# Optimization experiments

Hardware: AMD Instinct MI355X
Metric: run time of the kernel (lower is better)

Reference implementation:

```python
import jax, jax.numpy as jnp
import numpy as np

WIDTH = 256
HEAD = 16
SCALE = 2
G = WIDTH // HEAD          # 16 groups
NH = G * SCALE             # 32 kernelized heads
EPS = 1e-5
N_NODES = 20000
B_GRAPHS = 1024


def setup_inputs() -> dict:
    key = jax.random.key(0)
    ks = jax.random.split(key, 10)
    x = jax.random.normal(ks[0], (N_NODES, WIDTH), jnp.float32)
    x_res = jax.random.normal(ks[1], (B_GRAPHS, NH, HEAD, HEAD), jnp.float32)
    batch = jnp.sort(jax.random.randint(ks[2], (N_NODES,), 0, B_GRAPHS)).astype(jnp.int64)
    w_pre = jax.random.normal(ks[3], (WIDTH, WIDTH), jnp.float32) * 0.02
    b_pre = jnp.zeros((WIDTH,), jnp.float32)
    # grouped 1x1 convs: [groups, width_scale, head_out, head_in]
    wq = jax.random.normal(ks[4], (G, SCALE, HEAD, HEAD), jnp.float32) * 0.02
    wk = jax.random.normal(ks[5], (G, SCALE, HEAD, HEAD), jnp.float32) * 0.02
    wv = jax.random.normal(ks[6], (G, SCALE, HEAD, HEAD), jnp.float32) * 0.02
    w_post = jax.random.normal(ks[7], (WIDTH, WIDTH * SCALE), jnp.float32) * 0.02
    b_post = jnp.zeros((WIDTH,), jnp.float32)
    log_scale = jnp.full((WIDTH,), np.log(0.01), jnp.float32)
    return {"x": x, "x_res": x_res, "batch": batch, "batch_size": B_GRAPHS,
            "w_pre": w_pre, "b_pre": b_pre, "wq": wq, "wk": wk, "wv": wv,
            "w_post": w_post, "b_post": b_post, "log_scale": log_scale}


def reference(x, x_res, batch, batch_size, w_pre, b_pre, wq, wk, wv, w_post, b_post, log_scale):
    n = x.shape[0]
    # pre: 1x1 conv (= linear) + GroupNorm(affine=False); L=1 so normalize over
    # each group's width_head channels.
    y = x @ w_pre.T + b_pre                       # [N, width]
    yg = y.reshape(n, G, HEAD)                    # [N, G, Hd]
    mu = yg.mean(-1, keepdims=True)
    var = yg.var(-1, keepdims=True)               # biased, as in GroupNorm
    yn = (yg - mu) / jnp.sqrt(var + EPS)          # [N, G, Hd]

    inv_sqrt_h = 1.0 / np.sqrt(HEAD)
    # grouped convs -> kernelized q,k (exp) and v
    xq = jnp.exp(jnp.einsum('ngi,gsoi->ngso', yn, wq) * inv_sqrt_h).reshape(n, NH, HEAD)
    xk = jnp.exp(jnp.einsum('ngi,gsoi->ngso', yn, wk) * inv_sqrt_h).reshape(n, NH, HEAD)
    xv = jnp.einsum('ngi,gsoi->ngso', yn, wv).reshape(n, NH, HEAD)

    # outer product k (x) v then scatter-sum over graphs  [B, NH, Hd, Hd]
    kv = jnp.einsum('bnh,bnv->bnhv', xk, xv)
    kv_sum = jax.ops.segment_sum(kv, batch, num_segments=batch_size) + x_res
    x_res_out = kv_sum

    # per-graph key sum, gathered back to nodes
    k_sum = jax.ops.segment_sum(xk, batch, num_segments=batch_size)[batch]  # [N, NH, Hd]
    denom = jnp.einsum('bnh,bnh->bn', xq, k_sum)                            # [N, NH]
    qn = xq / denom[:, :, None]

    out = jnp.einsum('bnh,bnhv->bnv', qn, kv_sum[batch]).reshape(n, WIDTH * SCALE)
    out = jnp.exp(log_scale) * (out @ w_post.T + b_post)                    # [N, width]
    return (out, x_res_out)
```

## Files before the change

### kernel.cpp

```cpp
#include <hip/hip_runtime.h>
#include <stdint.h>

typedef unsigned int u32;
typedef unsigned short u16;
typedef __attribute__((ext_vector_type(8))) short v8s;
typedef __attribute__((ext_vector_type(4))) float v4f;

#define GN_EPS 1e-5f

__device__ __forceinline__ float bflo(u32 u){ return __uint_as_float(u << 16); }
__device__ __forceinline__ float bfhi(u32 u){ return __uint_as_float(u & 0xffff0000u); }
__device__ __forceinline__ u16 f2bf(float f){
  u32 x = __float_as_uint(f);
  u32 r = (x + 0x7fffu + ((x >> 16) & 1u)) >> 16;
  return (u16)r;
}
__device__ __forceinline__ u32 pack2(float a, float b){
  return (u32)f2bf(a) | ((u32)f2bf(b) << 16);
}
__device__ __forceinline__ void unpack8(const uint4 u, float* f){
  f[0]=bflo(u.x); f[1]=bfhi(u.x); f[2]=bflo(u.y); f[3]=bfhi(u.y);
  f[4]=bflo(u.z); f[5]=bfhi(u.z); f[6]=bflo(u.w); f[7]=bfhi(u.w);
}
__device__ __forceinline__ uint4 loadpack8(const float* __restrict__ p){
  float4 a = *(const float4*)p, b = *(const float4*)(p + 4);
  return make_uint4(pack2(a.x,a.y),pack2(a.z,a.w),pack2(b.x,b.y),pack2(b.z,b.w));
}

__device__ __forceinline__ int getb(const int* __restrict__ b, int is64, int i){
  return b[is64 ? 2*i : i];
}

__global__ __launch_bounds__(256) void k_detect(
    const int* __restrict__ batch, int n, int* __restrict__ flags)
{
  int i = blockIdx.x*256 + threadIdx.x;
  int bad = 0;
  if (i < n - 1 && batch[i] > batch[i + 1]) bad = 1;
  if (__builtin_amdgcn_ballot_w64(bad) != 0 && (threadIdx.x & 63) == 0)
    atomicOr(&flags[0], 1);
}

__global__ __launch_bounds__(256) void k_bounds(
    const int* __restrict__ batch, const int* __restrict__ flags,
    int N, int B, int* __restrict__ bounds)
{
  int i = blockIdx.x*256 + threadIdx.x;
  if (i >= N) return;
  const int is64 = flags[0];
  int b = getb(batch, is64, i);
  int prev = (i == 0) ? -1 : getb(batch, is64, i - 1);
  for (int g = prev + 1; g <= b; g++) bounds[g] = i;
  if (i == N - 1)
    for (int g = b + 1; g <= B; g++) bounds[g] = N;
}

__global__ __launch_bounds__(256) void k_pre(
    const float* __restrict__ x, const float* __restrict__ wpre,
    const float* __restrict__ bpre, u16* __restrict__ y, int N, int nbm)
{
  __shared__ __align__(16) u16 As[128*40];
  __shared__ __align__(16) u16 Bs[64*40];
  const int t = threadIdx.x;
  const int bm = blockIdx.x % nbm;
  const int bn = blockIdx.x / nbm;
  const int m_base = bm*128, n_base = bn*64;
  const int w = t >> 6, lane = t & 63;
  const int wr = (w >> 1)*64, wc = (w & 1)*32;
  const int fr = lane & 15, fk = lane >> 4;
  const int arow = t >> 1, acol = (t & 1)*16;
  const int brow = t >> 2, bcol = (t & 3)*8;

  v4f acc[4][2];
#pragma unroll
  for (int i = 0; i < 4; i++)
#pragma unroll
    for (int j = 0; j < 2; j++) acc[i][j] = (v4f){0.f,0.f,0.f,0.f};

  for (int k0 = 0; k0 < 256; k0 += 32) {
    __syncthreads();
    {
      int gm = m_base + arow;
      uint4 a0 = make_uint4(0u,0u,0u,0u), a1 = make_uint4(0u,0u,0u,0u);
      if (gm < N) {
        a0 = loadpack8(x + (size_t)gm*256 + k0 + acol);
        a1 = loadpack8(x + (size_t)gm*256 + k0 + acol + 8);
      }
      *(uint4*)&As[arow*40 + acol]     = a0;
      *(uint4*)&As[arow*40 + acol + 8] = a1;
      uint4 bv = loadpack8(wpre + (size_t)(n_base + brow)*256 + k0 + bcol);
      *(uint4*)&Bs[brow*40 + bcol] = bv;
    }
    __syncthreads();
    v8s b0 = *(const v8s*)&Bs[(wc      + fr)*40 + fk*8];
    v8s b1 = *(const v8s*)&Bs[(wc + 16 + fr)*40 + fk*8];
#pragma unroll
    for (int mi = 0; mi < 4; mi++) {
      v8s a = *(const v8s*)&As[(wr + mi*16 + fr)*40 + fk*8];
      acc[mi][0] = __builtin_amdgcn_mfma_f32_16x16x32_bf16(a,b0,acc[mi][0],0,0,0);
      acc[mi][1] = __builtin_amdgcn_mfma_f32_16x16x32_bf16(a,b1,acc[mi][1],0,0,0);
    }
  }
#pragma unroll
  for (int nj = 0; nj < 2; nj++) {
    int col = n_base + wc + nj*16 + fr;
    float bpv = bpre[col];
#pragma unroll
    for (int mi = 0; mi < 4; mi++) {
#pragma unroll
      for (int r = 0; r < 4; r++) {
        int row = m_base + wr + mi*16 + fk*4 + r;
        if (row < N) y[(size_t)row*256 + col] = f2bf(acc[mi][nj][r] + bpv);
      }
    }
  }
}

__global__ __launch_bounds__(256) void k_gnqkv(
    const u16* __restrict__ y, const float* __restrict__ wq,
    const float* __restrict__ wk, const float* __restrict__ wv,
    u16* __restrict__ qo, u16* __restrict__ ko, u16* __restrict__ vo, int N)
{
  __shared__ __align__(16) float wL[3*512];
  const int t = threadIdx.x;
  const int g = blockIdx.x & 15;
  const int c = blockIdx.x >> 4;
  {
    const float* srcs[3] = {wq, wk, wv};
#pragma unroll
    for (int tz = 0; tz < 3; tz++) {
      wL[tz*512 + t]       = srcs[tz][g*512 + t];
      wL[tz*512 + t + 256] = srcs[tz][g*512 + t + 256];
    }
  }
  __syncthreads();
  const int node = c*256 + t;
  if (node >= N) return;

  const u16* yp = y + (size_t)node*256 + g*16;
  uint4 Y0 = *(const uint4*)yp;
  uint4 Y1 = *(const uint4*)(yp + 8);
  float a[16]; unpack8(Y0, a); unpack8(Y1, a + 8);
  float mu = 0.f;
#pragma unroll
  for (int i = 0; i < 16; i++) mu += a[i];
  mu *= 0.0625f;
  float s2 = 0.f;
#pragma unroll
  for (int i = 0; i < 16; i++) { float d = a[i]-mu; s2 = fmaf(d,d,s2); }
  float inv = rsqrtf(s2*0.0625f + GN_EPS);
  float yn[16];
#pragma unroll
  for (int i = 0; i < 16; i++) yn[i] = (a[i]-mu)*inv;

  u16* outs[3] = {qo, ko, vo};
#pragma unroll
  for (int tz = 0; tz < 3; tz++) {
#pragma unroll
    for (int s = 0; s < 2; s++) {
      u32 p[8];
#pragma unroll
      for (int o = 0; o < 16; o++) {
        const float* row = &wL[tz*512 + (s*16 + o)*16];
        float4 W0 = *(const float4*)row;
        float4 W1 = *(const float4*)(row + 4);
        float4 W2 = *(const float4*)(row + 8);
        float4 W3 = *(const float4*)(row + 12);
        float w[16] = {W0.x,W0.y,W0.z,W0.w,W1.x,W1.y,W1.z,W1.w,
                       W2.x,W2.y,W2.z,W2.w,W3.x,W3.y,W3.z,W3.w};
        float d = 0.f;
#pragma unroll
        for (int i = 0; i < 16; i++) d = fmaf(yn[i], w[i], d);
        if (tz < 2) d = __expf(d*0.25f);
        if (o & 1) p[o>>1] |= (u32)f2bf(d) << 16;
        else       p[o>>1]  = (u32)f2bf(d);
      }
      u16* dst = outs[tz] + (size_t)node*512 + g*32 + s*16;
      *(uint4*)dst       = make_uint4(p[0],p[1],p[2],p[3]);
      *(uint4*)(dst + 8) = make_uint4(p[4],p[5],p[6],p[7]);
    }
  }
}

__global__ __launch_bounds__(512) void k_segatt(
    const u16* __restrict__ xk, const u16* __restrict__ xv,
    const u16* __restrict__ xq, const float* __restrict__ xres,
    const int* __restrict__ bounds,
    float* __restrict__ out1, u16* __restrict__ att, int N)
{
  __shared__ __align__(16) float red[512*20];
  __shared__ __align__(16) float kspart[512];
  __shared__ __align__(16) u16 kvs[32*280];
  __shared__ float kss[32*17];
  const int b = blockIdx.x, t = threadIdx.x;
  const int lo = bounds[b], hi = bounds[b+1];
  const int half = t >> 8;
  const int nh = (t >> 3) & 31, hp = t & 7;

  float kv[2][16];
#pragma unroll
  for (int r = 0; r < 2; r++)
#pragma unroll
    for (int v = 0; v < 16; v++) kv[r][v] = 0.f;
  float ks0 = 0.f, ks1 = 0.f;

  const size_t koff = (size_t)nh*16 + 2*hp;
  const size_t voff = (size_t)nh*16;
  int node = lo + half;
  for (; node + 2 < hi; node += 4) {
    u32  kw0 = *(const u32*) (xk + (size_t)node*512 + koff);
    uint4 Va0 = *(const uint4*)(xv + (size_t)node*512 + voff);
    uint4 Va1 = *(const uint4*)(xv + (size_t)node*512 + voff + 8);
    u32  kw1 = *(const u32*) (xk + (size_t)(node+2)*512 + koff);
    uint4 Vb0 = *(const uint4*)(xv + (size_t)(node+2)*512 + voff);
    uint4 Vb1 = *(const uint4*)(xv + (size_t)(node+2)*512 + voff + 8);
    float a0 = bflo(kw0), a1 = bfhi(kw0);
    float b0 = bflo(kw1), b1 = bfhi(kw1);
    float va[16], vb[16];
    unpack8(Va0, va); unpack8(Va1, va + 8);
    unpack8(Vb0, vb); unpack8(Vb1, vb + 8);
    ks0 += a0 + b0; ks1 += a1 + b1;
#pragma unroll
    for (int v = 0; v < 16; v++) {
      kv[0][v] = fmaf(a0, va[v], kv[0][v]);
      kv[1][v] = fmaf(a1, va[v], kv[1][v]);
      kv[0][v] = fmaf(b0, vb[v], kv[0][v]);
      kv[1][v] = fmaf(b1, vb[v], kv[1][v]);
    }
  }
  if (node < hi) {
    u32  kw = *(const u32*) (xk + (size_t)node*512 + koff);
    uint4 V0 = *(const uint4*)(xv + (size_t)node*512 + voff);
    uint4 V1 = *(const uint4*)(xv + (size_t)node*512 + voff + 8);
    float k0 = bflo(kw), k1 = bfhi(kw);
    float vf[16]; unpack8(V0, vf); unpack8(V1, vf + 8);
    ks0 += k0; ks1 += k1;
#pragma unroll
    for (int v = 0; v < 16; v++) {
      kv[0][v] = fmaf(k0, vf[v], kv[0][v]);
      kv[1][v] = fmaf(k1, vf[v], kv[1][v]);
    }
  }

  if (half == 0) {
#pragma unroll
    for (int r = 0; r < 2; r++) {
      float* rp = &red[(nh*16 + 2*hp + r)*20];
      *(float4*)rp       = make_float4(kv[r][0], kv[r][1], kv[r][2], kv[r][3]);
      *(float4*)(rp + 4) = make_float4(kv[r][4], kv[r][5], kv[r][6], kv[r][7]);
      *(float4*)(rp + 8) = make_float4(kv[r][8], kv[r][9], kv[r][10],kv[r][11]);
      *(float4*)(rp + 12)= make_float4(kv[r][12],kv[r][13],kv[r][14],kv[r][15]);
    }
    kspart[nh*16 + 2*hp]     = ks0;
    kspart[nh*16 + 2*hp + 1] = ks1;
  }
  __syncthreads();

  if (half == 1) {
#pragma unroll
    for (int r = 0; r < 2; r++) {
      const float* rp = &red[(nh*16 + 2*hp + r)*20];
      float4 R0 = *(const float4*)rp;
      float4 R1 = *(const float4*)(rp + 4);
      float4 R2 = *(const float4*)(rp + 8);
      float4 R3 = *(const float4*)(rp + 12);
      kv[r][0] += R0.x; kv[r][1] += R0.y; kv[r][2] += R0.z; kv[r][3] += R0.w;
      kv[r][4] += R1.x; kv[r][5] += R1.y; kv[r][6] += R1.z; kv[r][7] += R1.w;
      kv[r][8] += R2.x; kv[r][9] += R2.y; kv[r][10]+= R2.z; kv[r][11]+= R2.w;
      kv[r][12]+= R3.x; kv[r][13]+= R3.y; kv[r][14]+= R3.z; kv[r][15]+= R3.w;
    }
    ks0 += kspart[nh*16 + 2*hp];
    ks1 += kspart[nh*16 + 2*hp + 1];
    kss[nh*17 + 2*hp]     = ks0;
    kss[nh*17 + 2*hp + 1] = ks1;

#pragma unroll
    for (int r = 0; r < 2; r++) {
      int h = 2*hp + r;
      size_t idx = ((size_t)(b*32 + nh)*16 + h)*16;
      const float* xp = xres + idx;
      float4 X0 = *(const float4*)xp;
      float4 X1 = *(const float4*)(xp + 4);
      float4 X2 = *(const float4*)(xp + 8);
      float4 X3 = *(const float4*)(xp + 12);
      float xf[16] = {X0.x,X0.y,X0.z,X0.w,X1.x,X1.y,X1.z,X1.w,
                      X2.x,X2.y,X2.z,X2.w,X3.x,X3.y,X3.z,X3.w};
      float o[16];
#pragma unroll
      for (int j = 0; j < 16; j++) o[j] = kv[r][j] + xf[j];
      float* op = out1 + idx;
      *(float4*)op        = make_float4(o[0],o[1],o[2],o[3]);
      *(float4*)(op + 4)  = make_float4(o[4],o[5],o[6],o[7]);
      *(float4*)(op + 8)  = make_float4(o[8],o[9],o[10],o[11]);
      *(float4*)(op + 12) = make_float4(o[12],o[13],o[14],o[15]);
      u16* lp = &kvs[nh*280 + h*16];
      *(uint4*)lp       = make_uint4(pack2(o[0],o[1]),  pack2(o[2],o[3]),
                                     pack2(o[4],o[5]),  pack2(o[6],o[7]));
      *(uint4*)(lp + 8) = make_uint4(pack2(o[8],o[9]),  pack2(o[10],o[11]),
                                     pack2(o[12],o[13]),pack2(o[14],o[15]));
    }
  }
  __syncthreads();

  const int nh2 = t & 31, ns = t >> 5;
  for (int n0 = lo; n0 < hi; n0 += 16) {
    int nodei = n0 + ns;
    if (nodei >= hi) continue;
    const u16* qp = xq + (size_t)nodei*512 + nh2*16;
    uint4 Q0 = *(const uint4*)qp;
    uint4 Q1 = *(const uint4*)(qp + 8);
    float q[16]; unpack8(Q0, q); unpack8(Q1, q + 8);
    const float* ksp = &kss[nh2*17];
    float denom = 0.f;
#pragma unroll
    for (int i = 0; i < 16; i++) denom = fmaf(q[i], ksp[i], denom);
    float inv = 1.0f / fmaxf(denom, 1e-20f);
    float a[16];
#pragma unroll
    for (int v = 0; v < 16; v++) a[v] = 0.f;
    const u16* kvp = &kvs[nh2*280];
#pragma unroll
    for (int h = 0; h < 16; h++) {
      float qh = q[h] * inv;
      uint4 W0 = *(const uint4*)(kvp + h*16);
      uint4 W1 = *(const uint4*)(kvp + h*16 + 8);
      float w[16]; unpack8(W0, w); unpack8(W1, w + 8);
#pragma unroll
      for (int v = 0; v < 16; v++) a[v] = fmaf(qh, w[v], a[v]);
    }
    u32 p[8];
#pragma unroll
    for (int j = 0; j < 8; j++) p[j] = pack2(a[2*j], a[2*j+1]);
    u16* dst = att + (size_t)nodei*512 + nh2*16;
    *(uint4*)dst       = make_uint4(p[0],p[1],p[2],p[3]);
    *(uint4*)(dst + 8) = make_uint4(p[4],p[5],p[6],p[7]);
  }
}

__global__ __launch_bounds__(256) void k_post(
    const u16* __restrict__ att, const float* __restrict__ wpost,
    const float* __restrict__ bpost, const float* __restrict__ ls,
    float* __restrict__ out0, int N, int nbm)
{
  __shared__ __align__(16) u16 As[128*40];
  __shared__ __align__(16) u16 Bs[64*40];
  const int t = threadIdx.x;
  const int bm = blockIdx.x % nbm;
  const int bn = blockIdx.x / nbm;
  const int m_base = bm*128, n_base = bn*64;
  const int w = t >> 6, lane = t & 63;
  const int wr = (w >> 1)*64, wc = (w & 1)*32;
  const int fr = lane & 15, fk = lane >> 4;
  const int arow = t >> 1, acol = (t & 1)*16;
  const int brow = t >> 2, bcol = (t & 3)*8;

  v4f acc[4][2];
#pragma unroll
  for (int i = 0; i < 4; i++)
#pragma unroll
    for (int j = 0; j < 2; j++) acc[i][j] = (v4f){0.f,0.f,0.f,0.f};

  for (int k0 = 0; k0 < 512; k0 += 32) {
    __syncthreads();
    {
      int gm = m_base + arow;
      uint4 a0 = make_uint4(0u,0u,0u,0u), a1 = make_uint4(0u,0u,0u,0u);
      if (gm < N) {
        a0 = *(const uint4*)(att + (size_t)gm*512 + k0 + acol);
        a1 = *(const uint4*)(att + (size_t)gm*512 + k0 + acol + 8);
      }
      *(uint4*)&As[arow*40 + acol]     = a0;
      *(uint4*)&As[arow*40 + acol + 8] = a1;
      uint4 bv = loadpack8(wpost + (size_t)(n_base + brow)*512 + k0 + bcol);
      *(uint4*)&Bs[brow*40 + bcol] = bv;
    }
    __syncthreads();
    v8s b0 = *(const v8s*)&Bs[(wc      + fr)*40 + fk*8];
    v8s b1 = *(const v8s*)&Bs[(wc + 16 + fr)*40 + fk*8];
#pragma unroll
    for (int mi = 0; mi < 4; mi++) {
      v8s a = *(const v8s*)&As[(wr + mi*16 + fr)*40 + fk*8];
      acc[mi][0] = __builtin_amdgcn_mfma_f32_16x16x32_bf16(a,b0,acc[mi][0],0,0,0);
      acc[mi][1] = __builtin_amdgcn_mfma_f32_16x16x32_bf16(a,b1,acc[mi][1],0,0,0);
    }
  }
#pragma unroll
  for (int nj = 0; nj < 2; nj++) {
    int col = n_base + wc + nj*16 + fr;
    float bpv = bpost[col];
    float e   = __expf(ls[col]);
#pragma unroll
    for (int mi = 0; mi < 4; mi++) {
#pragma unroll
      for (int r = 0; r < 4; r++) {
        int row = m_base + wr + mi*16 + fk*4 + r;
        if (row < N) out0[(size_t)row*256 + col] = e*(acc[mi][nj][r] + bpv);
      }
    }
  }
}

extern "C" void kernel_launch(void* const* d_in, const int* in_sizes, int n_in,
                              void* d_out, int out_size, void* d_ws, size_t ws_size,
                              hipStream_t stream)
{
  const float* x     = (const float*)d_in[0];
  const float* xres  = (const float*)d_in[1];
  const int*   batch = (const int*)d_in[2];
  const float* wpre  = (const float*)d_in[4];
  const float* bpre  = (const float*)d_in[5];
  const float* wq    = (const float*)d_in[6];
  const float* wk    = (const float*)d_in[7];
  const float* wv    = (const float*)d_in[8];
  const float* wpost = (const float*)d_in[9];
  const float* bpost = (const float*)d_in[10];
  const float* ls    = (const float*)d_in[11];

  const int N = in_sizes[0] / 256;
  const int B = in_sizes[1] / 8192;
  const int nbm = (N + 127) / 128;
  const int nchunk = (N + 255) / 256;

  char* ws = (char*)d_ws;
  size_t off = 0;
  int*   flags  = (int*)(ws + off); off += 256;
  int*   bounds = (int*)(ws + off); off += ((size_t)B + 64) * 4;
  u16*   y      = (u16*)(ws + off);  off += (size_t)N * 512;
  u16*   att    = (u16*)(ws + off);  off += (size_t)N * 1024;
  u16*   q      = (u16*)(ws + off);  off += (size_t)N * 1024;
  u16*   kten   = (u16*)(ws + off);  off += (size_t)N * 1024;
  u16*   vten   = (u16*)(ws + off);  off += (size_t)N * 1024;

  float* out0 = (float*)d_out;
  float* out1 = out0 + (size_t)N * 256;

  hipMemsetAsync(flags, 0, 4, stream);
  k_detect<<<nchunk,         256, 0, stream>>>(batch, N, flags);
  k_bounds<<<nchunk,         256, 0, stream>>>(batch, flags, N, B, bounds);
  k_pre   <<<nbm * 4,        256, 0, stream>>>(x, wpre, bpre, y, N, nbm);
  k_gnqkv <<<nchunk * 16,    256, 0, stream>>>(y, wq, wk, wv, q, kten, vten, N);
  k_segatt<<<B,              512, 0, stream>>>(kten, vten, q, xres, bounds,
                                               out1, att, N);
  k_post  <<<nbm * 4,        256, 0, stream>>>(att, wpost, bpost, ls, out0, N, nbm);
}
```

Baseline: 133.1 us.

## Remap segment KV reduction to one row per thread, drop shared-memory split reduction

The per-graph KV accumulation no longer splits nodes across two thread halves that are later combined through a 40KB shared reduction buffer. Each of the 512 threads now owns one (head, key-dim) row and walks every node of the graph, so the shared buffers and one barrier disappear. This frees LDS, which may allow more resident blocks, and removes the cross-half combine step. In exchange each thread runs twice as many serial node iterations, and the key loads become 2-byte scalar reads instead of paired 4-byte reads.

```diff
diff --git a/kernel.cpp b/kernel.cpp
--- a/kernel.cpp
+++ b/kernel.cpp
@@ -10,6 +10,7 @@
 
 __device__ __forceinline__ float bflo(u32 u){ return __uint_as_float(u << 16); }
 __device__ __forceinline__ float bfhi(u32 u){ return __uint_as_float(u & 0xffff0000u); }
+__device__ __forceinline__ float bf1(u16 u){ return __uint_as_float((u32)u << 16); }
 __device__ __forceinline__ u16 f2bf(float f){
   u32 x = __float_as_uint(f);
   u32 r = (x + 0x7fffu + ((x >> 16) & 1u)) >> 16;
@@ -188,117 +189,73 @@
     const int* __restrict__ bounds,
     float* __restrict__ out1, u16* __restrict__ att, int N)
 {
-  __shared__ __align__(16) float red[512*20];
-  __shared__ __align__(16) float kspart[512];
   __shared__ __align__(16) u16 kvs[32*280];
   __shared__ float kss[32*17];
   const int b = blockIdx.x, t = threadIdx.x;
   const int lo = bounds[b], hi = bounds[b+1];
-  const int half = t >> 8;
-  const int nh = (t >> 3) & 31, hp = t & 7;
-
-  float kv[2][16];
-#pragma unroll
-  for (int r = 0; r < 2; r++)
-#pragma unroll
-    for (int v = 0; v < 16; v++) kv[r][v] = 0.f;
-  float ks0 = 0.f, ks1 = 0.f;
-
-  const size_t koff = (size_t)nh*16 + 2*hp;
+  const int nh = t >> 4, d = t & 15;
+
+  float kv[16];
+#pragma unroll
+  for (int v = 0; v < 16; v++) kv[v] = 0.f;
+  float ks = 0.f;
+
+  const size_t koff = (size_t)nh*16 + d;
   const size_t voff = (size_t)nh*16;
-  int node = lo + half;
-  for (; node + 2 < hi; node += 4) {
-    u32  kw0 = *(const u32*) (xk + (size_t)node*512 + koff);
+  int node = lo;
+  for (; node + 1 < hi; node += 2) {
+    u16  ka  = xk[(size_t)node*512 + koff];
     uint4 Va0 = *(const uint4*)(xv + (size_t)node*512 + voff);
     uint4 Va1 = *(const uint4*)(xv + (size_t)node*512 + voff + 8);
-    u32  kw1 = *(const u32*) (xk + (size_t)(node+2)*512 + koff);
-    uint4 Vb0 = *(const uint4*)(xv + (size_t)(node+2)*512 + voff);
-    uint4 Vb1 = *(const uint4*)(xv + (size_t)(node+2)*512 + voff + 8);
-    float a0 = bflo(kw0), a1 = bfhi(kw0);
-    float b0 = bflo(kw1), b1 = bfhi(kw1);
+    u16  kb  = xk[(size_t)(node+1)*512 + koff];
+    uint4 Vb0 = *(const uint4*)(xv + (size_t)(node+1)*512 + voff);
+    uint4 Vb1 = *(const uint4*)(xv + (size_t)(node+1)*512 + voff + 8);
+    float k0 = bf1(ka), k1 = bf1(kb);
     float va[16], vb[16];
     unpack8(Va0, va); unpack8(Va1, va + 8);
     unpack8(Vb0, vb); unpack8(Vb1, vb + 8);
-    ks0 += a0 + b0; ks1 += a1 + b1;
+    ks += k0 + k1;
 #pragma unroll
     for (int v = 0; v < 16; v++) {
-      kv[0][v] = fmaf(a0, va[v], kv[0][v]);
-      kv[1][v] = fmaf(a1, va[v], kv[1][v]);
-      kv[0][v] = fmaf(b0, vb[v], kv[0][v]);
-      kv[1][v] = fmaf(b1, vb[v], kv[1][v]);
+      kv[v] = fmaf(k0, va[v], kv[v]);
+      kv[v] = fmaf(k1, vb[v], kv[v]);
     }
   }
   if (node < hi) {
-    u32  kw = *(const u32*) (xk + (size_t)node*512 + koff);
+    u16  ka  = xk[(size_t)node*512 + koff];
     uint4 V0 = *(const uint4*)(xv + (size_t)node*512 + voff);
     uint4 V1 = *(const uint4*)(xv + (size_t)node*512 + voff + 8);
-    float k0 = bflo(kw), k1 = bfhi(kw);
+    float k0 = bf1(ka);
     float vf[16]; unpack8(V0, vf); unpack8(V1, vf + 8);
-    ks0 += k0; ks1 += k1;
-#pragma unroll
-    for (int v = 0; v < 16; v++) {
-      kv[0][v] = fmaf(k0, vf[v], kv[0][v]);
-      kv[1][v] = fmaf(k1, vf[v], kv[1][v]);
-    }
-  }
-
-  if (half == 0) {
-#pragma unroll
-    for (int r = 0; r < 2; r++) {
-      float* rp = &red[(nh*16 + 2*hp + r)*20];
-      *(float4*)rp       = make_float4(kv[r][0], kv[r][1], kv[r][2], kv[r][3]);
-      *(float4*)(rp + 4) = make_float4(kv[r][4], kv[r][5], kv[r][6], kv[r][7]);
-      *(float4*)(rp + 8) = make_float4(kv[r][8], kv[r][9], kv[r][10],kv[r][11]);
-      *(float4*)(rp + 12)= make_float4(kv[r][12],kv[r][13],kv[r][14],kv[r][15]);
-    }
-    kspart[nh*16 + 2*hp]     = ks0;
-    kspart[nh*16 + 2*hp + 1] = ks1;
-  }
-  __syncthreads();
-
-  if (half == 1) {
-#pragma unroll
-    for (int r = 0; r < 2; r++) {
-      const float* rp = &red[(nh*16 + 2*hp + r)*20];
-      float4 R0 = *(const float4*)rp;
-      float4 R1 = *(const float4*)(rp + 4);
-      float4 R2 = *(const float4*)(rp + 8);
-      float4 R3 = *(const float4*)(rp + 12);
-      kv[r][0] += R0.x; kv[r][1] += R0.y; kv[r][2] += R0.z; kv[r][3] += R0.w;
-      kv[r][4] += R1.x; kv[r][5] += R1.y; kv[r][6] += R1.z; kv[r][7] += R1.w;
-      kv[r][8] += R2.x; kv[r][9] += R2.y; kv[r][10]+= R2.z; kv[r][11]+= R2.w;
-      kv[r][12]+= R3.x; kv[r][13]+= R3.y; kv[r][14]+= R3.z; kv[r][15]+= R3.w;
-    }
-    ks0 += kspart[nh*16 + 2*hp];
-    ks1 += kspart[nh*16 + 2*hp + 1];
-    kss[nh*17 + 2*hp]     = ks0;
-    kss[nh*17 + 2*hp + 1] = ks1;
-
-#pragma unroll
-    for (int r = 0; r < 2; r++) {
-      int h = 2*hp + r;
-      size_t idx = ((size_t)(b*32 + nh)*16 + h)*16;
-      const float* xp = xres + idx;
-      float4 X0 = *(const float4*)xp;
-      float4 X1 = *(const float4*)(xp + 4);
-      float4 X2 = *(const float4*)(xp + 8);
-      float4 X3 = *(const float4*)(xp + 12);
-      float xf[16] = {X0.x,X0.y,X0.z,X0.w,X1.x,X1.y,X1.z,X1.w,
-                      X2.x,X2.y,X2.z,X2.w,X3.x,X3.y,X3.z,X3.w};
-      float o[16];
-#pragma unroll
-      for (int j = 0; j < 16; j++) o[j] = kv[r][j] + xf[j];
-      float* op = out1 + idx;
-      *(float4*)op        = make_float4(o[0],o[1],o[2],o[3]);
-      *(float4*)(op + 4)  = make_float4(o[4],o[5],o[6],o[7]);
-      *(float4*)(op + 8)  = make_float4(o[8],o[9],o[10],o[11]);
-      *(float4*)(op + 12) = make_float4(o[12],o[13],o[14],o[15]);
-      u16* lp = &kvs[nh*280 + h*16];
-      *(uint4*)lp       = make_uint4(pack2(o[0],o[1]),  pack2(o[2],o[3]),
-                                     pack2(o[4],o[5]),  pack2(o[6],o[7]));
-      *(uint4*)(lp + 8) = make_uint4(pack2(o[8],o[9]),  pack2(o[10],o[11]),
-                                     pack2(o[12],o[13]),pack2(o[14],o[15]));
-    }
+    ks += k0;
+#pragma unroll
+    for (int v = 0; v < 16; v++) kv[v] = fmaf(k0, vf[v], kv[v]);
+  }
+
+  kss[nh*17 + d] = ks;
+
+  {
+    size_t idx = ((size_t)(b*32 + nh)*16 + d)*16;
+    const float* xp = xres + idx;
+    float4 X0 = *(const float4*)xp;
+    float4 X1 = *(const float4*)(xp + 4);
+    float4 X2 = *(const float4*)(xp + 8);
+    float4 X3 = *(const float4*)(xp + 12);
+    float xf[16] = {X0.x,X0.y,X0.z,X0.w,X1.x,X1.y,X1.z,X1.w,
+                    X2.x,X2.y,X2.z,X2.w,X3.x,X3.y,X3.z,X3.w};
+    float o[16];
+#pragma unroll
+    for (int j = 0; j < 16; j++) o[j] = kv[j] + xf[j];
+    float* op = out1 + idx;
+    *(float4*)op        = make_float4(o[0],o[1],o[2],o[3]);
+    *(float4*)(op + 4)  = make_float4(o[4],o[5],o[6],o[7]);
+    *(float4*)(op + 8)  = make_float4(o[8],o[9],o[10],o[11]);
+    *(float4*)(op + 12) = make_float4(o[12],o[13],o[14],o[15]);
+    u16* lp = &kvs[nh*280 + d*16];
+    *(uint4*)lp       = make_uint4(pack2(o[0],o[1]),  pack2(o[2],o[3]),
+                                   pack2(o[4],o[5]),  pack2(o[6],o[7]));
+    *(uint4*)(lp + 8) = make_uint4(pack2(o[8],o[9]),  pack2(o[10],o[11]),
+                                   pack2(o[12],o[13]),pack2(o[14],o[15]));
   }
   __syncthreads();
 
```

Result: no change. 130.8 us (-1.8%).
